# Kernel optimization log

Hardware: AMD Instinct MI355X
Metric: run time of the kernel (lower is better)

The kernel has to match this reference:

```python
import jax, jax.numpy as jnp
import numpy as np

B, C, H, W, K = 8, 256, 128, 128, 19  # batch, image channels, spatial, num keypoints


def _uniform_linear(key, out_dim, in_dim):
    # torch nn.Linear default init: U(-1/sqrt(fan_in), 1/sqrt(fan_in))
    bound = 1.0 / np.sqrt(in_dim)
    kw, kb = jax.random.split(key)
    w = jax.random.uniform(kw, (out_dim, in_dim), jnp.float32, -bound, bound)
    b = jax.random.uniform(kb, (out_dim,), jnp.float32, -bound, bound)
    return w, b


def setup_inputs() -> dict:
    key = jax.random.key(0)
    ks = jax.random.split(key, 8)
    image_features = jax.random.normal(ks[0], (B, C, H, W), jnp.float32)
    # keypoints: (x, y, vis). forward computes int((x / W).clamp(0, W-1)), so
    # coords are drawn in [0, W*W) / [0, H*H) to cover the full heatmap grid.
    kx = jax.random.uniform(ks[1], (B, K), jnp.float32, 0.0, float(W * W))
    ky = jax.random.uniform(ks[2], (B, K), jnp.float32, 0.0, float(H * H))
    vis = jax.random.uniform(ks[3], (B, K), jnp.float32)  # >0 => visible
    keypoint_features = jnp.stack([kx, ky, vis], axis=-1)  # [B,K,3]
    img_fc_w, img_fc_b = _uniform_linear(ks[4], C, C)
    kp_proj_w, kp_proj_b = _uniform_linear(ks[5], K, K)  # 1x1 conv == K->K linear over channels
    kp_fc_w, kp_fc_b = _uniform_linear(ks[6], C, K)
    attn_fc_w, attn_fc_b = _uniform_linear(ks[7], 1, C)
    return {
        "image_features": image_features,
        "keypoint_features": keypoint_features,
        "img_fc_w": img_fc_w, "img_fc_b": img_fc_b,
        "kp_proj_w": kp_proj_w, "kp_proj_b": kp_proj_b,
        "kp_fc_w": kp_fc_w, "kp_fc_b": kp_fc_b,
        "attn_fc_w": attn_fc_w, "attn_fc_b": attn_fc_b,
    }


def keypoints_to_heatmap(keypoints, Hh, Ww):
    # Vectorized version of the original nested Python double-loop scatter.
    bsz, nkp, _ = keypoints.shape
    vis = (keypoints[:, :, 2] > 0).astype(jnp.float32)            # [B,K]
    # clamp to [0, dim-1] then truncate to int (values are >=0 so floor==trunc)
    x = jnp.clip(keypoints[:, :, 0] / Ww, 0.0, Ww - 1).astype(jnp.int32)  # [B,K]
    y = jnp.clip(keypoints[:, :, 1] / Hh, 0.0, Hh - 1).astype(jnp.int32)  # [B,K]
    bi = jnp.arange(bsz)[:, None]
    ki = jnp.arange(nkp)[None, :]
    heatmap = jnp.zeros((bsz, nkp, Hh, Ww), jnp.float32)
    # one write per (b,k) -> indices unique across writes; add of 0 for invisible kp
    return heatmap.at[bi, ki, y, x].add(vis)


def reference(image_features, keypoint_features,
              img_fc_w, img_fc_b, kp_proj_w, kp_proj_b,
              kp_fc_w, kp_fc_b, attn_fc_w, attn_fc_b):
    bsz, nch, Hh, Ww = image_features.shape
    heatmap = keypoints_to_heatmap(keypoint_features, Hh, Ww)  # [B,K,H,W]
    # F.interpolate to the same (H,W) with bilinear/align_corners=False maps
    # output pixel i -> input coord i exactly => identity; no-op.
    # keypoint_proj: 1x1 conv over K channels == per-pixel K->K linear
    kp_feat = jnp.einsum('bkhw,ok->bohw', heatmap, kp_proj_w) + kp_proj_b[None, :, None, None]
    img = image_features.reshape(bsz, nch, Hh * Ww).transpose(0, 2, 1)   # [B,S,C]
    kp = kp_feat.reshape(bsz, K, Hh * Ww).transpose(0, 2, 1)             # [B,S,K]
    img_proj = jnp.einsum('bsc,oc->bso', img, img_fc_w) + img_fc_b       # [B,S,C]
    kp_proj = jnp.einsum('bsk,ok->bso', kp, kp_fc_w) + kp_fc_b           # [B,S,C]
    combined = jnp.tanh(img_proj + kp_proj)
    scores = jax.nn.sigmoid(jnp.einsum('bsc,oc->bso', combined, attn_fc_w) + attn_fc_b)  # [B,S,1]
    attended = img * scores                                              # [B,S,C]
    return attended.transpose(0, 2, 1).reshape(bsz, nch, Hh, Ww)
```

## Files before the change

### kernel.cpp

```cpp
#include <hip/hip_runtime.h>
#include <hip/hip_bf16.h>

#define CCH 256
#define HH 128
#define WW 128
#define SS (HH*WW)
#define NB 8
#define NK 19
#define STILE 32
#define NTIL (NB * (SS / STILE))

typedef __attribute__((ext_vector_type(8))) short short8v;
typedef __attribute__((ext_vector_type(4))) float f32x4;
typedef __attribute__((ext_vector_type(2))) float f32x2;

static __device__ __forceinline__ unsigned short f2bf(float x) {
    __hip_bfloat16 h = __float2bfloat16(x);
    return *reinterpret_cast<unsigned short*>(&h);
}
static __device__ __forceinline__ float bf2f(unsigned short u) {
    union { unsigned int i; float f; } z; z.i = ((unsigned int)u) << 16; return z.f;
}
static __device__ __forceinline__ float tanh_fast(float x) {
    float e = __expf(2.f * x);
    return 1.f - 2.f * __builtin_amdgcn_rcpf(e + 1.f);
}
static __device__ __forceinline__ float sigmoid_fast(float z) {
    return __builtin_amdgcn_rcpf(1.f + __expf(-z));
}
static __device__ __forceinline__ void gload_lds16(const float* g, float* l) {
    __builtin_amdgcn_global_load_lds(
        (const __attribute__((address_space(1))) void*)g,
        (__attribute__((address_space(3))) void*)l, 16, 0, 0);
}

__global__ __launch_bounds__(256) void precompute_kernel(
    const float* __restrict__ kf,
    const float* __restrict__ img_fc_w,
    const float* __restrict__ img_fc_b,
    const float* __restrict__ kp_proj_w,
    const float* __restrict__ kp_proj_b,
    const float* __restrict__ kp_fc_w,
    const float* __restrict__ kp_fc_b,
    float* __restrict__ cb,
    float* __restrict__ delta,
    int* __restrict__ pix,
    unsigned short* __restrict__ Wfrag)
{
    int t = threadIdx.x;
    {
        float acc = img_fc_b[t] + kp_fc_b[t];
        for (int k2 = 0; k2 < NK; ++k2) acc += kp_fc_w[t * NK + k2] * kp_proj_b[k2];
        cb[t] = acc;
        for (int k = 0; k < NK; ++k) {
            float d = 0.f;
            for (int k2 = 0; k2 < NK; ++k2) d += kp_fc_w[t * NK + k2] * kp_proj_w[k2 * NK + k];
            delta[t * NK + k] = d;
        }
    }
    if (t < NB * NK) {
        float kx = kf[t * 3 + 0], ky = kf[t * 3 + 1], vis = kf[t * 3 + 2];
        int p = -1;
        if (vis > 0.f) {
            int xi = (int)fminf(fmaxf(kx * (1.f / (float)WW), 0.f), (float)(WW - 1));
            int yi = (int)fminf(fmaxf(ky * (1.f / (float)HH), 0.f), (float)(HH - 1));
            p = yi * WW + xi;
        }
        pix[t] = p;
    }
    for (int g = t; g < 8 * 16 * 64; g += 256) {
        int lane = g & 63;
        int ot = (g >> 6) & 15;
        int ks = g >> 10;
        int o = ot * 16 + (lane & 15);
        int c0 = ks * 32 + (lane >> 4) * 8;
#pragma unroll
        for (int j = 0; j < 8; ++j)
            Wfrag[g * 8 + j] = f2bf(img_fc_w[o * CCH + c0 + j]);
    }
}

__global__ __launch_bounds__(512, 4) void main_kernel(
    const float* __restrict__ img,
    const unsigned short* __restrict__ Wfrag,
    const float* __restrict__ cb,
    const float* __restrict__ aw,
    const float* __restrict__ attn_b,
    float* __restrict__ out)
{
    __shared__ __align__(16) char smem[35840];
    float* Xf = reinterpret_cast<float*>(smem);
    unsigned short* Xl = reinterpret_cast<unsigned short*>(smem);
    float* partial = reinterpret_cast<float*>(smem + 32768);
    float* cbl = reinterpret_cast<float*>(smem + 33792);
    float* awl = reinterpret_cast<float*>(smem + 34816);

    const int t = threadIdx.x;
    const int l = t & 63;
    const int w = t >> 6;

    const int bid = blockIdx.x;
    const int swz = (bid & 7) * (NTIL / 8) + (bid >> 3);
    const int b = swz >> 9;
    const int sb = (swz & 511) * STILE;
    const float* imgb = img + (size_t)b * CCH * SS;

    short8v areg[2][8];
#pragma unroll
    for (int ks = 0; ks < 8; ++ks)
#pragma unroll
        for (int m = 0; m < 2; ++m)
            areg[m][ks] = *reinterpret_cast<const short8v*>(
                &Wfrag[(((ks * 16 + (w * 2 + m)) * 64) + l) * 8]);

#pragma unroll
    for (int i = 0; i < 4; ++i) {
        const int c0 = w * 32 + i * 8;
        gload_lds16(imgb + (size_t)(c0 + (l >> 3)) * SS + sb + (l & 7) * 4,
                    &Xf[c0 * STILE]);
    }

    if (t < 256) { cbl[t] = cb[t]; awl[t] = aw[t]; }
    __syncthreads();

    const int sl = t & 31;
    const int cg16 = (t >> 5) * 16;
    {
        float xv[16];
#pragma unroll
        for (int j = 0; j < 16; ++j) xv[j] = Xf[(cg16 + j) * STILE + sl];
        __syncthreads();
#pragma unroll
        for (int h = 0; h < 2; ++h) {
            short8v pk;
#pragma unroll
            for (int e = 0; e < 8; ++e) pk[e] = (short)f2bf(xv[h * 8 + e]);
            int cblk = (cg16 >> 3) + h;
            int idx = sl * 256 + ((cblk ^ (sl & 7)) << 3);
            *reinterpret_cast<short8v*>(&Xl[idx]) = pk;
        }
    }
    __syncthreads();

    f32x4 acc[2][2];
#pragma unroll
    for (int m = 0; m < 2; ++m)
#pragma unroll
        for (int n = 0; n < 2; ++n)
            acc[m][n] = (f32x4){0.f, 0.f, 0.f, 0.f};

#pragma unroll
    for (int ks = 0; ks < 8; ++ks) {
        const int cblk = ks * 4 + (l >> 4);
        const int s0 = (l & 15), s1 = 16 + (l & 15);
        short8v bf0 = *reinterpret_cast<const short8v*>(
            &Xl[s0 * 256 + ((cblk ^ (s0 & 7)) << 3)]);
        short8v bf1 = *reinterpret_cast<const short8v*>(
            &Xl[s1 * 256 + ((cblk ^ (s1 & 7)) << 3)]);
        acc[0][0] = __builtin_amdgcn_mfma_f32_16x16x32_bf16(areg[0][ks], bf0, acc[0][0], 0, 0, 0);
        acc[1][0] = __builtin_amdgcn_mfma_f32_16x16x32_bf16(areg[1][ks], bf0, acc[1][0], 0, 0, 0);
        acc[0][1] = __builtin_amdgcn_mfma_f32_16x16x32_bf16(areg[0][ks], bf1, acc[0][1], 0, 0, 0);
        acc[1][1] = __builtin_amdgcn_mfma_f32_16x16x32_bf16(areg[1][ks], bf1, acc[1][1], 0, 0, 0);
    }

    float p2[2];
#pragma unroll
    for (int n = 0; n < 2; ++n) {
        float accp = 0.f;
#pragma unroll
        for (int m = 0; m < 2; ++m)
#pragma unroll
            for (int r = 0; r < 4; ++r) {
                int o = (w * 2 + m) * 16 + ((l >> 4) << 2) + r;
                accp += awl[o] * tanh_fast(acc[m][n][r] + cbl[o]);
            }
        accp += __shfl_xor(accp, 16);
        accp += __shfl_xor(accp, 32);
        p2[n] = accp;
    }
    if (l < 16) {
        partial[w * STILE + l] = p2[0];
        partial[w * STILE + 16 + l] = p2[1];
    }
    __syncthreads();

    {
        const int pq = (t & 15) * 2;
        const int cg = t >> 4;
        const int c0 = cg * 8;
        const float ab = attn_b[0];
        float z0 = ab, z1 = ab;
#pragma unroll
        for (int ww = 0; ww < 8; ++ww) {
            z0 += partial[ww * STILE + pq];
            z1 += partial[ww * STILE + pq + 1];
        }
        float s0v = sigmoid_fast(z0);
        float s1v = sigmoid_fast(z1);

        short8v v0, v1;
        {
            int i0 = pq * 256 + ((cg ^ (pq & 7)) << 3);
            int i1 = (pq + 1) * 256 + ((cg ^ ((pq + 1) & 7)) << 3);
            v0 = *reinterpret_cast<const short8v*>(&Xl[i0]);
            v1 = *reinterpret_cast<const short8v*>(&Xl[i1]);
        }
#pragma unroll
        for (int j = 0; j < 8; ++j) {
            f32x2 o2;
            o2[0] = bf2f((unsigned short)v0[j]) * s0v;
            o2[1] = bf2f((unsigned short)v1[j]) * s1v;
            __builtin_nontemporal_store(o2, reinterpret_cast<f32x2*>(
                out + (size_t)(b * CCH + c0 + j) * SS + sb + pq));
        }
    }
}

__global__ __launch_bounds__(256) void fixup_kernel(
    const float* __restrict__ img,
    const float* __restrict__ img_fc_w,
    const float* __restrict__ aw,
    const float* __restrict__ attn_b,
    const float* __restrict__ cb,
    const float* __restrict__ delta,
    const int* __restrict__ pix,
    float* __restrict__ out)
{
    int bk = blockIdx.x;
    int b = bk / NK;
    int p = pix[bk];
    if (p < 0) return;
    __shared__ float x[256];
    __shared__ float red[256];
    __shared__ float ssc;
    int t = threadIdx.x;
    const float* imgb = img + (size_t)b * CCH * SS;
    x[t] = imgb[(size_t)t * SS + p];
    __syncthreads();
    float dsum = 0.f;
    for (int k2 = 0; k2 < NK; ++k2)
        if (pix[b * NK + k2] == p) dsum += delta[t * NK + k2];
    float acc = cb[t] + dsum;
    for (int c = 0; c < CCH; ++c) acc += img_fc_w[t * CCH + c] * x[c];
    red[t] = aw[t] * tanh_fast(acc);
    __syncthreads();
    for (int off = 128; off > 0; off >>= 1) {
        if (t < off) red[t] += red[t + off];
        __syncthreads();
    }
    if (t == 0) ssc = sigmoid_fast(red[0] + attn_b[0]);
    __syncthreads();
    __builtin_nontemporal_store(x[t] * ssc, out + (size_t)(b * CCH + t) * SS + p);
}

extern "C" void kernel_launch(void* const* d_in, const int* in_sizes, int n_in,
                              void* d_out, int out_size, void* d_ws, size_t ws_size,
                              hipStream_t stream) {
    (void)in_sizes; (void)n_in; (void)out_size; (void)ws_size;
    const float* img       = (const float*)d_in[0];
    const float* kf        = (const float*)d_in[1];
    const float* img_fc_w  = (const float*)d_in[2];
    const float* img_fc_b  = (const float*)d_in[3];
    const float* kp_proj_w = (const float*)d_in[4];
    const float* kp_proj_b = (const float*)d_in[5];
    const float* kp_fc_w   = (const float*)d_in[6];
    const float* kp_fc_b   = (const float*)d_in[7];
    const float* attn_fc_w = (const float*)d_in[8];
    const float* attn_fc_b = (const float*)d_in[9];
    float* out = (float*)d_out;

    char* ws = (char*)d_ws;
    float* cb             = (float*)(ws);
    float* delta          = (float*)(ws + 1024);
    int*   pix            = (int*)  (ws + 20480);
    unsigned short* Wfrag = (unsigned short*)(ws + 21504);

    precompute_kernel<<<1, 256, 0, stream>>>(kf, img_fc_w, img_fc_b, kp_proj_w,
                                             kp_proj_b, kp_fc_w, kp_fc_b,
                                             cb, delta, pix, Wfrag);
    main_kernel<<<NTIL, 512, 0, stream>>>(img, Wfrag, cb,
                                          attn_fc_w, attn_fc_b, out);
    fixup_kernel<<<NB * NK, 256, 0, stream>>>(img, img_fc_w, attn_fc_w, attn_fc_b,
                                              cb, delta, pix, out);
}
```

Before: 77.26 us.

## Make main kernel persistent over eight tiles with double-buffered async LDS loads

Each block now handles eight consecutive 32-pixel tiles instead of one. The next tile's image slice is prefetched into a second LDS buffer with direct global-to-LDS loads while the current tile runs its MFMA and epilogue, and explicit vmcnt waits plus barriers replace syncthreads. This amortises weight-fragment register loads and per-block setup, and hides global load latency. LDS use roughly doubles to about 67 KB per block, which can cut occupancy below the four blocks per CU requested in the launch bounds. The hand-written waitcnt values are fragile if the compiler adds or reorders vector memory operations.

```diff
diff --git a/kernel.cpp b/kernel.cpp
--- a/kernel.cpp
+++ b/kernel.cpp
@@ -8,7 +8,9 @@
 #define NB 8
 #define NK 19
 #define STILE 32
+#define TPB 8
 #define NTIL (NB * (SS / STILE))
+#define NBLK (NTIL / TPB)
 
 typedef __attribute__((ext_vector_type(8))) short short8v;
 typedef __attribute__((ext_vector_type(4))) float f32x4;
@@ -32,6 +34,10 @@
     __builtin_amdgcn_global_load_lds(
         (const __attribute__((address_space(1))) void*)g,
         (__attribute__((address_space(3))) void*)l, 16, 0, 0);
+}
+static __device__ __forceinline__ void lgkm0_fence() {
+    asm volatile("s_waitcnt lgkmcnt(0)" ::: "memory");
+    __builtin_amdgcn_sched_barrier(0);
 }
 
 __global__ __launch_bounds__(256) void precompute_kernel(
@@ -88,22 +94,23 @@
     const float* __restrict__ attn_b,
     float* __restrict__ out)
 {
-    __shared__ __align__(16) char smem[35840];
-    float* Xf = reinterpret_cast<float*>(smem);
-    unsigned short* Xl = reinterpret_cast<unsigned short*>(smem);
-    float* partial = reinterpret_cast<float*>(smem + 32768);
-    float* cbl = reinterpret_cast<float*>(smem + 33792);
-    float* awl = reinterpret_cast<float*>(smem + 34816);
+    __shared__ __align__(16) char smem[68608];
+    float* Xf0 = reinterpret_cast<float*>(smem);
+    float* Xf1 = reinterpret_cast<float*>(smem + 32768);
+    float* partial = reinterpret_cast<float*>(smem + 65536);
+    float* cbl = reinterpret_cast<float*>(smem + 66560);
+    float* awl = reinterpret_cast<float*>(smem + 67584);
 
     const int t = threadIdx.x;
     const int l = t & 63;
     const int w = t >> 6;
 
     const int bid = blockIdx.x;
-    const int swz = (bid & 7) * (NTIL / 8) + (bid >> 3);
-    const int b = swz >> 9;
-    const int sb = (swz & 511) * STILE;
-    const float* imgb = img + (size_t)b * CCH * SS;
+    const int swz = (bid & 7) * (NBLK / 8) + (bid >> 3);
+    const int tile0 = swz * TPB;
+    const float ab = attn_b[0];
+
+    if (t < 256) { cbl[t] = cb[t]; awl[t] = aw[t]; }
 
     short8v areg[2][8];
 #pragma unroll
@@ -113,82 +120,106 @@
             areg[m][ks] = *reinterpret_cast<const short8v*>(
                 &Wfrag[(((ks * 16 + (w * 2 + m)) * 64) + l) * 8]);
 
+    asm volatile("s_waitcnt vmcnt(0) lgkmcnt(0)" ::: "memory");
+    __builtin_amdgcn_sched_barrier(0);
+
 #pragma unroll
     for (int i = 0; i < 4; ++i) {
         const int c0 = w * 32 + i * 8;
-        gload_lds16(imgb + (size_t)(c0 + (l >> 3)) * SS + sb + (l & 7) * 4,
-                    &Xf[c0 * STILE]);
-    }
-
-    if (t < 256) { cbl[t] = cb[t]; awl[t] = aw[t]; }
-    __syncthreads();
+        {
+            const int tl = tile0;
+            const float* src = img + (size_t)(tl >> 9) * CCH * SS + (tl & 511) * STILE;
+            gload_lds16(src + (size_t)(c0 + (l >> 3)) * SS + (l & 7) * 4, &Xf0[c0 * STILE]);
+        }
+    }
+#pragma unroll
+    for (int i = 0; i < 4; ++i) {
+        const int c0 = w * 32 + i * 8;
+        {
+            const int tl = tile0 + 1;
+            const float* src = img + (size_t)(tl >> 9) * CCH * SS + (tl & 511) * STILE;
+            gload_lds16(src + (size_t)(c0 + (l >> 3)) * SS + (l & 7) * 4, &Xf1[c0 * STILE]);
+        }
+    }
 
     const int sl = t & 31;
     const int cg16 = (t >> 5) * 16;
-    {
+    const int pq = (t & 15) * 2;
+    const int cg = t >> 4;
+    const int c0s = cg * 8;
+
+    for (int it = 0; it < TPB; ++it) {
+        float* Xfc = (it & 1) ? Xf1 : Xf0;
+        unsigned short* Xl = reinterpret_cast<unsigned short*>(Xfc);
+        const int tile = tile0 + it;
+        const int b = tile >> 9;
+        const int sb = (tile & 511) * STILE;
+
+        if (it == 0)            asm volatile("s_waitcnt vmcnt(4)" ::: "memory");
+        else if (it == TPB - 1) asm volatile("s_waitcnt vmcnt(8)" ::: "memory");
+        else                    asm volatile("s_waitcnt vmcnt(12)" ::: "memory");
+        __builtin_amdgcn_sched_barrier(0);
+        __builtin_amdgcn_s_barrier();
+
         float xv[16];
 #pragma unroll
-        for (int j = 0; j < 16; ++j) xv[j] = Xf[(cg16 + j) * STILE + sl];
-        __syncthreads();
+        for (int j = 0; j < 16; ++j) xv[j] = Xfc[(cg16 + j) * STILE + sl];
+        lgkm0_fence();
+        __builtin_amdgcn_s_barrier();
+
 #pragma unroll
         for (int h = 0; h < 2; ++h) {
             short8v pk;
 #pragma unroll
             for (int e = 0; e < 8; ++e) pk[e] = (short)f2bf(xv[h * 8 + e]);
             int cblk = (cg16 >> 3) + h;
-            int idx = sl * 256 + ((cblk ^ (sl & 7)) << 3);
-            *reinterpret_cast<short8v*>(&Xl[idx]) = pk;
-        }
-    }
-    __syncthreads();
-
-    f32x4 acc[2][2];
-#pragma unroll
-    for (int m = 0; m < 2; ++m)
-#pragma unroll
-        for (int n = 0; n < 2; ++n)
-            acc[m][n] = (f32x4){0.f, 0.f, 0.f, 0.f};
-
-#pragma unroll
-    for (int ks = 0; ks < 8; ++ks) {
-        const int cblk = ks * 4 + (l >> 4);
-        const int s0 = (l & 15), s1 = 16 + (l & 15);
-        short8v bf0 = *reinterpret_cast<const short8v*>(
-            &Xl[s0 * 256 + ((cblk ^ (s0 & 7)) << 3)]);
-        short8v bf1 = *reinterpret_cast<const short8v*>(
-            &Xl[s1 * 256 + ((cblk ^ (s1 & 7)) << 3)]);
-        acc[0][0] = __builtin_amdgcn_mfma_f32_16x16x32_bf16(areg[0][ks], bf0, acc[0][0], 0, 0, 0);
-        acc[1][0] = __builtin_amdgcn_mfma_f32_16x16x32_bf16(areg[1][ks], bf0, acc[1][0], 0, 0, 0);
-        acc[0][1] = __builtin_amdgcn_mfma_f32_16x16x32_bf16(areg[0][ks], bf1, acc[0][1], 0, 0, 0);
-        acc[1][1] = __builtin_amdgcn_mfma_f32_16x16x32_bf16(areg[1][ks], bf1, acc[1][1], 0, 0, 0);
-    }
-
-    float p2[2];
-#pragma unroll
-    for (int n = 0; n < 2; ++n) {
-        float accp = 0.f;
+            *reinterpret_cast<short8v*>(&Xl[sl * 256 + ((cblk ^ (sl & 7)) << 3)]) = pk;
+        }
+        lgkm0_fence();
+        __builtin_amdgcn_s_barrier();
+
+        f32x4 acc[2][2];
 #pragma unroll
         for (int m = 0; m < 2; ++m)
 #pragma unroll
-            for (int r = 0; r < 4; ++r) {
-                int o = (w * 2 + m) * 16 + ((l >> 4) << 2) + r;
-                accp += awl[o] * tanh_fast(acc[m][n][r] + cbl[o]);
-            }
-        accp += __shfl_xor(accp, 16);
-        accp += __shfl_xor(accp, 32);
-        p2[n] = accp;
-    }
-    if (l < 16) {
-        partial[w * STILE + l] = p2[0];
-        partial[w * STILE + 16 + l] = p2[1];
-    }
-    __syncthreads();
-
-    {
-        const int pq = (t & 15) * 2;
-        const int cg = t >> 4;
-        const int c0 = cg * 8;
-        const float ab = attn_b[0];
+            for (int n = 0; n < 2; ++n)
+                acc[m][n] = (f32x4){0.f, 0.f, 0.f, 0.f};
+#pragma unroll
+        for (int ks = 0; ks < 8; ++ks) {
+            const int cblk = ks * 4 + (l >> 4);
+            const int s0 = l & 15, s1 = 16 + s0;
+            short8v bf0 = *reinterpret_cast<const short8v*>(
+                &Xl[s0 * 256 + ((cblk ^ (s0 & 7)) << 3)]);
+            short8v bf1 = *reinterpret_cast<const short8v*>(
+                &Xl[s1 * 256 + ((cblk ^ (s1 & 7)) << 3)]);
+            acc[0][0] = __builtin_amdgcn_mfma_f32_16x16x32_bf16(areg[0][ks], bf0, acc[0][0], 0, 0, 0);
+            acc[1][0] = __builtin_amdgcn_mfma_f32_16x16x32_bf16(areg[1][ks], bf0, acc[1][0], 0, 0, 0);
+            acc[0][1] = __builtin_amdgcn_mfma_f32_16x16x32_bf16(areg[0][ks], bf1, acc[0][1], 0, 0, 0);
+            acc[1][1] = __builtin_amdgcn_mfma_f32_16x16x32_bf16(areg[1][ks], bf1, acc[1][1], 0, 0, 0);
+        }
+
+        float p2[2];
+#pragma unroll
+        for (int n = 0; n < 2; ++n) {
+            float accp = 0.f;
+#pragma unroll
+            for (int m = 0; m < 2; ++m)
+#pragma unroll
+                for (int r = 0; r < 4; ++r) {
+                    int o = (w * 2 + m) * 16 + ((l >> 4) << 2) + r;
+                    accp += awl[o] * tanh_fast(acc[m][n][r] + cbl[o]);
+                }
+            accp += __shfl_xor(accp, 16);
+            accp += __shfl_xor(accp, 32);
+            p2[n] = accp;
+        }
+        if (l < 16) {
+            partial[w * STILE + l] = p2[0];
+            partial[w * STILE + 16 + l] = p2[1];
+        }
+        lgkm0_fence();
+        __builtin_amdgcn_s_barrier();
+
         float z0 = ab, z1 = ab;
 #pragma unroll
         for (int ww = 0; ww < 8; ++ww) {
@@ -197,21 +228,30 @@
         }
         float s0v = sigmoid_fast(z0);
         float s1v = sigmoid_fast(z1);
-
-        short8v v0, v1;
-        {
-            int i0 = pq * 256 + ((cg ^ (pq & 7)) << 3);
-            int i1 = (pq + 1) * 256 + ((cg ^ ((pq + 1) & 7)) << 3);
-            v0 = *reinterpret_cast<const short8v*>(&Xl[i0]);
-            v1 = *reinterpret_cast<const short8v*>(&Xl[i1]);
-        }
+        short8v v0 = *reinterpret_cast<const short8v*>(
+            &Xl[pq * 256 + ((cg ^ (pq & 7)) << 3)]);
+        short8v v1 = *reinterpret_cast<const short8v*>(
+            &Xl[(pq + 1) * 256 + ((cg ^ ((pq + 1) & 7)) << 3)]);
+        lgkm0_fence();
+        __builtin_amdgcn_s_barrier();
+
 #pragma unroll
         for (int j = 0; j < 8; ++j) {
             f32x2 o2;
             o2[0] = bf2f((unsigned short)v0[j]) * s0v;
             o2[1] = bf2f((unsigned short)v1[j]) * s1v;
             __builtin_nontemporal_store(o2, reinterpret_cast<f32x2*>(
-                out + (size_t)(b * CCH + c0 + j) * SS + sb + pq));
+                out + (size_t)(b * CCH + c0s + j) * SS + sb + pq));
+        }
+        if (it + 2 < TPB) {
+            const int tn = tile + 2;
+            const float* src = img + (size_t)(tn >> 9) * CCH * SS + (tn & 511) * STILE;
+#pragma unroll
+            for (int i = 0; i < 4; ++i) {
+                const int c0 = w * 32 + i * 8;
+                gload_lds16(src + (size_t)(c0 + (l >> 3)) * SS + (l & 7) * 4,
+                            &Xfc[c0 * STILE]);
+            }
         }
     }
 }
@@ -278,7 +318,7 @@
     precompute_kernel<<<1, 256, 0, stream>>>(kf, img_fc_w, img_fc_b, kp_proj_w,
                                              kp_proj_b, kp_fc_w, kp_fc_b,
                                              cb, delta, pix, Wfrag);
-    main_kernel<<<NTIL, 512, 0, stream>>>(img, Wfrag, cb,
+    main_kernel<<<NBLK, 512, 0, stream>>>(img, Wfrag, cb,
                                           attn_fc_w, attn_fc_b, out);
     fixup_kernel<<<NB * NK, 256, 0, stream>>>(img, img_fc_w, attn_fc_w, attn_fc_b,
                                               cb, delta, pix, out);
```

Result: slower. 117.4 us (+51.9%).
